# Kernel tuning notes

Measured on AMD Instinct MI355X. Metric: run time of the kernel, lower is better.

The kernel has to match this reference:

```python
import jax, jax.numpy as jnp
import numpy as np

N_NODES = 10000
N_EDGES = 80000
IN_DIM = 768
HID = 256
HEADS = 8
NEG_SLOPE = 0.2


def setup_inputs() -> dict:
    key = jax.random.key(0)
    ks = jax.random.split(key, 12)
    s = 0.02
    x = jax.random.normal(ks[0], (N_NODES, IN_DIM), dtype=jnp.float32)
    edge_index = jax.random.randint(ks[1], (2, N_EDGES), 0, N_NODES, dtype=jnp.int64)
    W1 = jax.random.normal(ks[2], (IN_DIM, HEADS * HID), dtype=jnp.float32) * s
    a_src1 = jax.random.normal(ks[3], (HEADS, HID), dtype=jnp.float32) * s
    a_dst1 = jax.random.normal(ks[4], (HEADS, HID), dtype=jnp.float32) * s
    b1 = jnp.zeros((HEADS * HID,), dtype=jnp.float32)
    W2 = jax.random.normal(ks[5], (HEADS * HID, HEADS * HID), dtype=jnp.float32) * s
    a_src2 = jax.random.normal(ks[6], (HEADS, HID), dtype=jnp.float32) * s
    a_dst2 = jax.random.normal(ks[7], (HEADS, HID), dtype=jnp.float32) * s
    b2 = jnp.zeros((HID,), dtype=jnp.float32)
    # graph_projection: 256 -> 256
    Wp = jax.random.normal(ks[8], (HID, HID), dtype=jnp.float32) * s
    bp = jnp.zeros((HID,), dtype=jnp.float32)
    return dict(x=x, edge_index=edge_index, W1=W1, a_src1=a_src1, a_dst1=a_dst1,
                b1=b1, W2=W2, a_src2=a_src2, a_dst2=a_dst2, b2=b2, Wp=Wp, bp=bp)


def _gat_conv(x, src, dst, W, a_src, a_dst, b, concat):
    """PyG GATConv (eval mode, self-loops already appended to src/dst)."""
    N = x.shape[0]
    H, C = a_src.shape
    h = (x @ W).reshape(N, H, C)                         # [N,H,C] per-head projection
    alpha_s = jnp.sum(h * a_src[None], axis=-1)           # [N,H]
    alpha_d = jnp.sum(h * a_dst[None], axis=-1)           # [N,H]
    e = jax.nn.leaky_relu(alpha_s[src] + alpha_d[dst], NEG_SLOPE)  # [E,H]
    # segment softmax over incoming edges of each dst node
    m = jax.ops.segment_max(e, dst, num_segments=N)       # [N,H]
    m = jnp.where(jnp.isfinite(m), m, 0.0)
    p = jnp.exp(e - m[dst])
    denom = jax.ops.segment_sum(p, dst, num_segments=N)   # [N,H]
    alpha = p / (denom[dst] + 1e-16)                      # [E,H]
    out = jax.ops.segment_sum(alpha[:, :, None] * h[src], dst, num_segments=N)  # [N,H,C]
    if concat:
        return out.reshape(N, H * C) + b
    return out.mean(axis=1) + b


def reference(x, edge_index, W1, a_src1, a_dst1, b1, W2, a_src2, a_dst2, b2, Wp, bp):
    N = x.shape[0]
    loops = jnp.arange(N, dtype=edge_index.dtype)
    src = jnp.concatenate([edge_index[0], loops])
    dst = jnp.concatenate([edge_index[1], loops])
    h = _gat_conv(x, src, dst, W1, a_src1, a_dst1, b1, concat=True)   # [N, 2048]
    h = jax.nn.elu(h)                                                 # dropout: eval/no-op
    h = _gat_conv(h, src, dst, W2, a_src2, a_dst2, b2, concat=False)  # [N, 256]
    h = h @ Wp + bp
    return jax.nn.relu(h)                                             # dropout: eval/no-op
```

## Files before the change

kernel.cpp:

```cpp
#include <hip/hip_runtime.h>
#include <cstdint>
#include <cstddef>

#define IN_DIM  768
#define NNODES  10000
#define MPAD    10112
#define NEDGES  80000
#define E_TOT   90000
#define HEADS   8
#define HID     256
#define HC      2048
#define NEG_SLOPE 0.2f

#define CVT_BLK  ((MPAD * IN_DIM / 4) / 256)
#define CNT_BLK  ((E_TOT + 255) / 256)
#define T1_BLK   ((HC / 32) * (IN_DIM / 32))
#define T2_BLK   ((HC / 32) * (HC / 32))
#define TP_BLK   ((HID / 32) * (HID / 32))
#define PREP_BLK (CVT_BLK + CNT_BLK + T1_BLK + T2_BLK + TP_BLK)

typedef _Float16 __attribute__((ext_vector_type(8))) f16x8;
typedef float    __attribute__((ext_vector_type(4))) f32x4;

__device__ __forceinline__ int edge_src(const int* __restrict__ ei, int e) {
    return (e < NEDGES) ? ei[e] : (e - NEDGES);
}
__device__ __forceinline__ int edge_dst(const int* __restrict__ ei, int e) {
    return (e < NEDGES) ? ei[NEDGES + e] : (e - NEDGES);
}

__device__ __forceinline__ void tcvt_body(
    const float* __restrict__ W, _Float16* __restrict__ T,
    int K, int N, int bx, int by, int t)
{
    __shared__ float tile[32][33];
    int tx = t & 31, ty = t >> 5;
#pragma unroll
    for (int q = 0; q < 4; q++)
        tile[ty + q * 8][tx] = W[(size_t)(by * 32 + ty + q * 8) * N + bx * 32 + tx];
    __syncthreads();
#pragma unroll
    for (int q = 0; q < 4; q++) {
        float v = tile[tx][ty + q * 8];
        T[(size_t)(bx * 32 + ty + q * 8) * K + by * 32 + tx] = (_Float16)v;
    }
}

__global__ __launch_bounds__(256) void prep_kernel(
    const float* __restrict__ x, _Float16* __restrict__ xh,
    const int* __restrict__ ei, int* __restrict__ cnt,
    const float* __restrict__ W1, _Float16* __restrict__ W1t,
    const float* __restrict__ W2, _Float16* __restrict__ W2t,
    const float* __restrict__ Wp, _Float16* __restrict__ Wpt)
{
    int b = blockIdx.x;
    int t = threadIdx.x;
    if (b < CVT_BLK) {
        int i = b * 256 + t;
        size_t e = (size_t)i * 4;
        int r = (int)(e / IN_DIM);
        float4 v = (r < NNODES) ? *(const float4*)(x + e)
                                : make_float4(0.f, 0.f, 0.f, 0.f);
        _Float16 h4[4] = {(_Float16)v.x, (_Float16)v.y, (_Float16)v.z, (_Float16)v.w};
        *(ushort4*)(xh + e) = *(ushort4*)h4;
    } else if (b < CVT_BLK + CNT_BLK) {
        int e = (b - CVT_BLK) * 256 + t;
        if (e < E_TOT) atomicAdd(&cnt[edge_dst(ei, e)], 1);
    } else if (b < CVT_BLK + CNT_BLK + T1_BLK) {
        int idx = b - (CVT_BLK + CNT_BLK);
        tcvt_body(W1, W1t, IN_DIM, HC, idx % (HC / 32), idx / (HC / 32), t);
    } else if (b < CVT_BLK + CNT_BLK + T1_BLK + T2_BLK) {
        int idx = b - (CVT_BLK + CNT_BLK + T1_BLK);
        tcvt_body(W2, W2t, HC, HC, idx % (HC / 32), idx / (HC / 32), t);
    } else {
        int idx = b - (CVT_BLK + CNT_BLK + T1_BLK + T2_BLK);
        tcvt_body(Wp, Wpt, HID, HID, idx % (HID / 32), idx / (HID / 32), t);
    }
}

__global__ void scan_kernel(const int* __restrict__ cnt, int* __restrict__ indptr) {
    __shared__ int sums[1024];
    const int CH = 10;
    int t = threadIdx.x;
    int base = t * CH;
    int s = 0;
#pragma unroll
    for (int i = 0; i < CH; i++) { int idx = base + i; if (idx < NNODES) s += cnt[idx]; }
    sums[t] = s;
    __syncthreads();
    for (int off = 1; off < 1024; off <<= 1) {
        int v = (t >= off) ? sums[t - off] : 0;
        __syncthreads();
        sums[t] += v;
        __syncthreads();
    }
    int run = (t == 0) ? 0 : sums[t - 1];
#pragma unroll
    for (int i = 0; i < CH; i++) {
        int idx = base + i;
        if (idx < NNODES) { indptr[idx] = run; run += cnt[idx]; }
    }
    if (t == 0) indptr[NNODES] = E_TOT;
}

__global__ void scatter_kernel(const int* __restrict__ ei, const int* __restrict__ indptr,
                               int* __restrict__ cur, int* __restrict__ sorted) {
    int e = blockIdx.x * 256 + threadIdx.x;
    if (e < E_TOT) {
        int d = edge_dst(ei, e);
        int pos = atomicAdd(&cur[d], 1);
        sorted[indptr[d] + pos] = e;
    }
}

template <int EPI>
__global__ __launch_bounds__(256) void mfma_gemm_kernel(
    const _Float16* __restrict__ A, const _Float16* __restrict__ B,
    void* __restrict__ Cout, const float* __restrict__ bias,
    int M, int K, int Nn, int swz)
{
    __shared__ __align__(16) _Float16 sA[2][128 * 32];
    __shared__ __align__(16) _Float16 sB[2][128 * 32];

    int t = threadIdx.x;
    int bx = blockIdx.x, by = blockIdx.y;
    if (swz) {
        int id = by * 16 + bx;
        int xcd = id & 7, slot = id >> 3;
        bx = 2 * xcd + (slot & 1);
        by = slot >> 1;
    }
    int row0 = by * 128;
    int col0 = bx * 128;

    int s0 = t, s1 = t + 256;
    int m0 = s0 >> 2, k0 = (s0 & 3) * 8;
    int m1 = s1 >> 2, k1 = (s1 & 3) * 8;
    const _Float16* a0 = A + (size_t)(row0 + m0) * K + k0;
    const _Float16* a1 = A + (size_t)(row0 + m1) * K + k1;
    const _Float16* b0 = B + (size_t)(col0 + m0) * K + k0;
    const _Float16* b1 = B + (size_t)(col0 + m1) * K + k1;

    int w = t >> 6, lane = t & 63;
    int wm = (w & 1) * 64, wn = (w >> 1) * 64;
    int fr = lane & 15, quad = lane >> 4;

    auto stage = [&](int kt, int bsel) {
        _Float16* dA0 = &sA[bsel][(w * 64) * 8];
        _Float16* dA1 = &sA[bsel][(w * 64 + 256) * 8];
        _Float16* dB0 = &sB[bsel][(w * 64) * 8];
        _Float16* dB1 = &sB[bsel][(w * 64 + 256) * 8];
        __builtin_amdgcn_global_load_lds(
            (const __attribute__((address_space(1))) void*)(a0 + kt),
            (__attribute__((address_space(3))) void*)dA0, 16, 0, 0);
        __builtin_amdgcn_global_load_lds(
            (const __attribute__((address_space(1))) void*)(a1 + kt),
            (__attribute__((address_space(3))) void*)dA1, 16, 0, 0);
        __builtin_amdgcn_global_load_lds(
            (const __attribute__((address_space(1))) void*)(b0 + kt),
            (__attribute__((address_space(3))) void*)dB0, 16, 0, 0);
        __builtin_amdgcn_global_load_lds(
            (const __attribute__((address_space(1))) void*)(b1 + kt),
            (__attribute__((address_space(3))) void*)dB1, 16, 0, 0);
    };

    f32x4 acc[4][4];
#pragma unroll
    for (int i = 0; i < 4; i++)
#pragma unroll
        for (int j = 0; j < 4; j++) acc[i][j] = {0.f, 0.f, 0.f, 0.f};

    const int nIt = K / 32;
    stage(0, 0);
    __syncthreads();

    for (int it = 0; it < nIt; ++it) {
        int cb = it & 1;
        if (it + 1 < nIt) stage((it + 1) * 32, cb ^ 1);

        f16x8 fa[4], fb[4];
#pragma unroll
        for (int i = 0; i < 4; i++) {
            fa[i] = *(const f16x8*)&sA[cb][(wm + i * 16 + fr) * 32 + quad * 8];
            fb[i] = *(const f16x8*)&sB[cb][(wn + i * 16 + fr) * 32 + quad * 8];
        }
#pragma unroll
        for (int i = 0; i < 4; i++)
#pragma unroll
            for (int j = 0; j < 4; j++)
                acc[i][j] = __builtin_amdgcn_mfma_f32_16x16x32_f16(fa[i], fb[j], acc[i][j], 0, 0, 0);

        if (it + 1 < nIt) __syncthreads();
    }

    if (EPI == 0) {
        _Float16* C = (_Float16*)Cout;
#pragma unroll
        for (int i = 0; i < 4; i++) {
            int mbase = row0 + wm + i * 16 + quad * 4;
#pragma unroll
            for (int j = 0; j < 4; j++) {
                int n = col0 + wn + j * 16 + fr;
#pragma unroll
                for (int r = 0; r < 4; r++) {
                    int m = mbase + r;
                    if (m < M) C[(size_t)m * Nn + n] = (_Float16)acc[i][j][r];
                }
            }
        }
    } else {
        float* C = (float*)Cout;
        float bv[4];
#pragma unroll
        for (int j = 0; j < 4; j++) bv[j] = bias[col0 + wn + j * 16 + fr];
#pragma unroll
        for (int i = 0; i < 4; i++) {
            int mbase = row0 + wm + i * 16 + quad * 4;
#pragma unroll
            for (int j = 0; j < 4; j++) {
                int n = col0 + wn + j * 16 + fr;
#pragma unroll
                for (int r = 0; r < 4; r++) {
                    int m = mbase + r;
                    if (m < M) C[(size_t)m * Nn + n] = fmaxf(acc[i][j][r] + bv[j], 0.f);
                }
            }
        }
    }
}

__global__ __launch_bounds__(256) void attn_kernel(
    const _Float16* __restrict__ H, const float* __restrict__ a_src,
    const float* __restrict__ a_dst, float* __restrict__ as_out,
    float* __restrict__ ad_out)
{
    int n = blockIdx.x;
    int t = threadIdx.x;
    int h = t >> 5, l = t & 31;
    f16x8 hv = *(const f16x8*)&H[(size_t)n * HC + h * HID + l * 8];
    const float* asp = a_src + h * HID + l * 8;
    const float* adp = a_dst + h * HID + l * 8;
    float sa = 0.f, sd = 0.f;
#pragma unroll
    for (int q = 0; q < 8; q++) {
        float v = (float)hv[q];
        sa = fmaf(v, asp[q], sa);
        sd = fmaf(v, adp[q], sd);
    }
#pragma unroll
    for (int o = 16; o > 0; o >>= 1) {
        sa += __shfl_xor(sa, o, 32);
        sd += __shfl_xor(sd, o, 32);
    }
    if (l == 0) { as_out[n * HEADS + h] = sa; ad_out[n * HEADS + h] = sd; }
}

template <int MODE>
__global__ __launch_bounds__(256) void agg_kernel(
    const _Float16* __restrict__ H, const float* __restrict__ as_,
    const float* __restrict__ ad_, const float* __restrict__ bias,
    const int* __restrict__ indptr, const int* __restrict__ sorted,
    const int* __restrict__ ei, _Float16* __restrict__ outh)
{
    __shared__ float m8[HEADS], d8[HEADS], adl[HEADS];
    __shared__ int   srcl[64];
    __shared__ float al[64][HEADS];
    __shared__ float red[HC];

    int n = blockIdx.x;
    int t = threadIdx.x;

    if (n >= NNODES) {
        if (MODE == 0) {
            _Float16 z8[8] = {};
            *(f16x8*)&outh[(size_t)n * HC + t * 8] = *(f16x8*)z8;
        } else {
            outh[(size_t)n * HID + t] = (_Float16)0.f;
        }
        return;
    }

    int start = indptr[n];
    int deg = indptr[n + 1] - start;

    if (t < HEADS) adl[t] = ad_[n * HEADS + t];
    __syncthreads();

    int h = t >> 5, l = t & 31;
    float adh = adl[h];

    float mx = -1e30f;
    for (int j = l; j < deg; j += 32) {
        int e = sorted[start + j];
        int s = edge_src(ei, e);
        float v = as_[s * HEADS + h] + adh;
        v = (v >= 0.f) ? v : NEG_SLOPE * v;
        mx = fmaxf(mx, v);
    }
#pragma unroll
    for (int o = 16; o > 0; o >>= 1) mx = fmaxf(mx, __shfl_xor(mx, o, 32));

    float sm = 0.f;
    for (int j = l; j < deg; j += 32) {
        int e = sorted[start + j];
        int s = edge_src(ei, e);
        float v = as_[s * HEADS + h] + adh;
        v = (v >= 0.f) ? v : NEG_SLOPE * v;
        sm += expf(v - mx);
    }
#pragma unroll
    for (int o = 16; o > 0; o >>= 1) sm += __shfl_xor(sm, o, 32);
    if (l == 0) { m8[h] = mx; d8[h] = sm; }

    int hh = t >> 5, c8 = (t & 31) * 8;
    const size_t hoff = (size_t)hh * HID + c8;
    float acc[8] = {};
    for (int base = 0; base < deg; base += 64) {
        int cntc = min(64, deg - base);
        __syncthreads();
        if (t < cntc) srcl[t] = edge_src(ei, sorted[start + base + t]);
        __syncthreads();
        {
            int j = t & 63, h0 = t >> 6;
            if (j < cntc) {
#pragma unroll
                for (int q = 0; q < 2; q++) {
                    int hx = h0 + q * 4;
                    float v = as_[srcl[j] * HEADS + hx] + adl[hx];
                    v = (v >= 0.f) ? v : NEG_SLOPE * v;
                    al[j][hx] = expf(v - m8[hx]) / (d8[hx] + 1e-16f);
                }
            }
        }
        __syncthreads();
        for (int jj = 0; jj < cntc; jj++) {
            int s = srcl[jj];
            f16x8 hv = *(const f16x8*)&H[(size_t)s * HC + hoff];
            float a = al[jj][hh];
#pragma unroll
            for (int q = 0; q < 8; q++)
                acc[q] = fmaf(a, (float)hv[q], acc[q]);
        }
    }

    if (MODE == 0) {
        _Float16 o8[8];
#pragma unroll
        for (int q = 0; q < 8; q++) {
            float v = acc[q] + bias[hoff + q];
            v = (v > 0.f) ? v : expm1f(v);
            o8[q] = (_Float16)v;
        }
        *(f16x8*)&outh[(size_t)n * HC + hoff] = *(f16x8*)o8;
    } else {
#pragma unroll
        for (int q = 0; q < 8; q++) red[hoff + q] = acc[q];
        __syncthreads();
        float s = 0.f;
#pragma unroll
        for (int h2 = 0; h2 < HEADS; h2++) s += red[h2 * HID + t];
        outh[(size_t)n * HID + t] = (_Float16)(s * 0.125f + bias[t]);
    }
}

extern "C" void kernel_launch(void* const* d_in, const int* in_sizes, int n_in,
                              void* d_out, int out_size, void* d_ws, size_t ws_size,
                              hipStream_t stream)
{
    const float* x      = (const float*)d_in[0];
    const int*   ei     = (const int*)  d_in[1];
    const float* W1     = (const float*)d_in[2];
    const float* a_src1 = (const float*)d_in[3];
    const float* a_dst1 = (const float*)d_in[4];
    const float* b1     = (const float*)d_in[5];
    const float* W2     = (const float*)d_in[6];
    const float* a_src2 = (const float*)d_in[7];
    const float* a_dst2 = (const float*)d_in[8];
    const float* b2     = (const float*)d_in[9];
    const float* Wp     = (const float*)d_in[10];
    const float* bp     = (const float*)d_in[11];
    float* out = (float*)d_out;

    char* ws = (char*)d_ws;
    size_t off = 0;
    auto alloc = [&](size_t bytes) -> char* {
        char* p = ws + off;
        off += (bytes + 255) & ~(size_t)255;
        return p;
    };
    _Float16* Hbuf = (_Float16*)alloc((size_t)NNODES * HC * 2);
    _Float16* A2   = (_Float16*)alloc((size_t)MPAD * HC * 2);
    _Float16* W1t  = (_Float16*)alloc((size_t)HC * IN_DIM * 2);
    _Float16* W2t  = (_Float16*)alloc((size_t)HC * HC * 2);
    _Float16* Wpt  = (_Float16*)alloc((size_t)HID * HID * 2);
    _Float16* xh   = (_Float16*)alloc((size_t)MPAD * IN_DIM * 2);
    _Float16* out2h = (_Float16*)alloc((size_t)MPAD * HID * 2);
    float* asad   = (float*)alloc((size_t)4 * NNODES * HEADS * sizeof(float));
    float* as1 = asad;
    float* ad1 = asad + (size_t)NNODES * HEADS;
    float* as2 = asad + (size_t)2 * NNODES * HEADS;
    float* ad2 = asad + (size_t)3 * NNODES * HEADS;
    int*   cntcur = (int*)alloc((size_t)2 * NNODES * sizeof(int));
    int*   cnt = cntcur;
    int*   cur = cntcur + NNODES;
    int*   indptr = (int*)  alloc((size_t)(NNODES + 1) * sizeof(int));
    int*   sorted = (int*)  alloc((size_t)E_TOT * sizeof(int));

    hipMemsetAsync(cntcur, 0, (size_t)2 * NNODES * sizeof(int), stream);
    prep_kernel<<<PREP_BLK, 256, 0, stream>>>(x, xh, ei, cnt,
                                              W1, W1t, W2, W2t, Wp, Wpt);
    scan_kernel<<<1, 1024, 0, stream>>>(cnt, indptr);
    scatter_kernel<<<(E_TOT + 255) / 256, 256, 0, stream>>>(ei, indptr, cur, sorted);

    dim3 gMf(HC / 128, MPAD / 128);

    mfma_gemm_kernel<0><<<gMf, 256, 0, stream>>>(xh, W1t, Hbuf, nullptr,
                                                 NNODES, IN_DIM, HC, 1);
    attn_kernel<<<NNODES, 256, 0, stream>>>(Hbuf, a_src1, a_dst1, as1, ad1);
    agg_kernel<0><<<MPAD, 256, 0, stream>>>(Hbuf, as1, ad1, b1, indptr, sorted, ei, A2);

    mfma_gemm_kernel<0><<<gMf, 256, 0, stream>>>(A2, W2t, Hbuf, nullptr,
                                                 NNODES, HC, HC, 1);
    attn_kernel<<<NNODES, 256, 0, stream>>>(Hbuf, a_src2, a_dst2, as2, ad2);
    agg_kernel<1><<<MPAD, 256, 0, stream>>>(Hbuf, as2, ad2, b2, indptr, sorted, ei, out2h);

    dim3 gProj(HID / 128, MPAD / 128);
    mfma_gemm_kernel<1><<<gProj, 256, 0, stream>>>(out2h, Wpt, out, bp,
                                                   NNODES, HID, HID, 0);
}
```

Measured before the change: 455.8 us.

## Fold attention-coefficient dot products into GEMM via precombined weight columns

Precomputes W·a_src and W·a_dst per head as 16 extra B-matrix rows (padded to a 128-column tile), so each GAT GEMM emits alpha_s/alpha_d in an extra column block and the separate attn_kernel passes over H are removed. The attention logits now come from fp16-rounded combined weights instead of dot products over the fp16 H, which shifts numerics slightly. It also drops the XCD block swizzle in the GEMM, and the extra column tile adds roughly 1/16 more GEMM blocks, mostly wasted MFMA work.

```diff
diff --git a/kernel.cpp b/kernel.cpp
--- a/kernel.cpp
+++ b/kernel.cpp
@@ -11,13 +11,19 @@
 #define HID     256
 #define HC      2048
 #define NEG_SLOPE 0.2f
+#define BROWS   (HC + 128)
 
 #define CVT_BLK  ((MPAD * IN_DIM / 4) / 256)
 #define CNT_BLK  ((E_TOT + 255) / 256)
 #define T1_BLK   ((HC / 32) * (IN_DIM / 32))
 #define T2_BLK   ((HC / 32) * (HC / 32))
 #define TP_BLK   ((HID / 32) * (HID / 32))
-#define PREP_BLK (CVT_BLK + CNT_BLK + T1_BLK + T2_BLK + TP_BLK)
+#define WC1_BLK  (16 * (IN_DIM / 128))
+#define WC2_BLK  (16 * (HC / 128))
+#define Z1_BLK   (112 * IN_DIM / 2048)
+#define Z2_BLK   (112 * HC / 2048)
+#define PREP_BLK (CVT_BLK + CNT_BLK + T1_BLK + T2_BLK + TP_BLK + \
+                  WC1_BLK + WC2_BLK + Z1_BLK + Z2_BLK)
 
 typedef _Float16 __attribute__((ext_vector_type(8))) f16x8;
 typedef float    __attribute__((ext_vector_type(4))) f32x4;
@@ -43,6 +49,28 @@
     for (int q = 0; q < 4; q++) {
         float v = tile[tx][ty + q * 8];
         T[(size_t)(bx * 32 + ty + q * 8) * K + by * 32 + tx] = (_Float16)v;
+    }
+}
+
+__device__ __forceinline__ void wcomb_body(
+    const float* __restrict__ W, const float* __restrict__ a,
+    _Float16* __restrict__ T, int K, int h16, int ktile, int t)
+{
+    int h = h16 & 7;
+    const float* av = a + h * HID;
+    int w = t >> 6, lane = t & 63;
+    float ar[4];
+#pragma unroll
+    for (int q = 0; q < 4; q++) ar[q] = av[lane + 64 * q];
+    for (int kk = w; kk < 128; kk += 4) {
+        int k = ktile * 128 + kk;
+        const float* wp = W + (size_t)k * HC + h * HID;
+        float s = 0.f;
+#pragma unroll
+        for (int q = 0; q < 4; q++) s = fmaf(wp[lane + 64 * q], ar[q], s);
+#pragma unroll
+        for (int o = 32; o > 0; o >>= 1) s += __shfl_xor(s, o, 64);
+        if (lane == 0) T[(size_t)(HC + h16) * K + k] = (_Float16)s;
     }
 }
 
@@ -51,11 +79,14 @@
     const int* __restrict__ ei, int* __restrict__ cnt,
     const float* __restrict__ W1, _Float16* __restrict__ W1t,
     const float* __restrict__ W2, _Float16* __restrict__ W2t,
-    const float* __restrict__ Wp, _Float16* __restrict__ Wpt)
+    const float* __restrict__ Wp, _Float16* __restrict__ Wpt,
+    const float* __restrict__ as1, const float* __restrict__ ad1,
+    const float* __restrict__ as2, const float* __restrict__ ad2)
 {
     int b = blockIdx.x;
     int t = threadIdx.x;
-    if (b < CVT_BLK) {
+    int base = 0;
+    if (b < (base += CVT_BLK)) {
         int i = b * 256 + t;
         size_t e = (size_t)i * 4;
         int r = (int)(e / IN_DIM);
@@ -63,18 +94,52 @@
                                 : make_float4(0.f, 0.f, 0.f, 0.f);
         _Float16 h4[4] = {(_Float16)v.x, (_Float16)v.y, (_Float16)v.z, (_Float16)v.w};
         *(ushort4*)(xh + e) = *(ushort4*)h4;
-    } else if (b < CVT_BLK + CNT_BLK) {
-        int e = (b - CVT_BLK) * 256 + t;
+        return;
+    }
+    if (b < (base += CNT_BLK)) {
+        int e = (b - (base - CNT_BLK)) * 256 + t;
         if (e < E_TOT) atomicAdd(&cnt[edge_dst(ei, e)], 1);
-    } else if (b < CVT_BLK + CNT_BLK + T1_BLK) {
-        int idx = b - (CVT_BLK + CNT_BLK);
+        return;
+    }
+    if (b < (base += T1_BLK)) {
+        int idx = b - (base - T1_BLK);
         tcvt_body(W1, W1t, IN_DIM, HC, idx % (HC / 32), idx / (HC / 32), t);
-    } else if (b < CVT_BLK + CNT_BLK + T1_BLK + T2_BLK) {
-        int idx = b - (CVT_BLK + CNT_BLK + T1_BLK);
+        return;
+    }
+    if (b < (base += T2_BLK)) {
+        int idx = b - (base - T2_BLK);
         tcvt_body(W2, W2t, HC, HC, idx % (HC / 32), idx / (HC / 32), t);
-    } else {
-        int idx = b - (CVT_BLK + CNT_BLK + T1_BLK + T2_BLK);
+        return;
+    }
+    if (b < (base += TP_BLK)) {
+        int idx = b - (base - TP_BLK);
         tcvt_body(Wp, Wpt, HID, HID, idx % (HID / 32), idx / (HID / 32), t);
+        return;
+    }
+    if (b < (base += WC1_BLK)) {
+        int idx = b - (base - WC1_BLK);
+        int h16 = idx / (IN_DIM / 128), ktile = idx % (IN_DIM / 128);
+        wcomb_body(W1, (h16 < 8) ? as1 : ad1, W1t, IN_DIM, h16, ktile, t);
+        return;
+    }
+    if (b < (base += WC2_BLK)) {
+        int idx = b - (base - WC2_BLK);
+        int h16 = idx / (HC / 128), ktile = idx % (HC / 128);
+        wcomb_body(W2, (h16 < 8) ? as2 : ad2, W2t, HC, h16, ktile, t);
+        return;
+    }
+    if (b < (base += Z1_BLK)) {
+        int idx = b - (base - Z1_BLK);
+        _Float16 z8[8] = {};
+        size_t e = (size_t)(HC + 16) * IN_DIM + (size_t)idx * 2048 + t * 8;
+        *(f16x8*)&W1t[e] = *(f16x8*)z8;
+        return;
+    }
+    {
+        int idx = b - base;
+        _Float16 z8[8] = {};
+        size_t e = (size_t)(HC + 16) * HC + (size_t)idx * 2048 + t * 8;
+        *(f16x8*)&W2t[e] = *(f16x8*)z8;
     }
 }
 
@@ -117,21 +182,14 @@
 __global__ __launch_bounds__(256) void mfma_gemm_kernel(
     const _Float16* __restrict__ A, const _Float16* __restrict__ B,
     void* __restrict__ Cout, const float* __restrict__ bias,
-    int M, int K, int Nn, int swz)
+    float* __restrict__ asad, int M, int K, int Nn)
 {
     __shared__ __align__(16) _Float16 sA[2][128 * 32];
     __shared__ __align__(16) _Float16 sB[2][128 * 32];
 
     int t = threadIdx.x;
-    int bx = blockIdx.x, by = blockIdx.y;
-    if (swz) {
-        int id = by * 16 + bx;
-        int xcd = id & 7, slot = id >> 3;
-        bx = 2 * xcd + (slot & 1);
-        by = slot >> 1;
-    }
-    int row0 = by * 128;
-    int col0 = bx * 128;
+    int row0 = blockIdx.y * 128;
+    int col0 = blockIdx.x * 128;
 
     int s0 = t, s1 = t + 256;
     int m0 = s0 >> 2, k0 = (s0 & 3) * 8;
@@ -193,6 +251,20 @@
         if (it + 1 < nIt) __syncthreads();
     }
 
+    if (EPI == 0 && col0 >= Nn) {
+        if (wn == 0) {
+#pragma unroll
+            for (int i = 0; i < 4; i++) {
+                int mbase = row0 + wm + i * 16 + quad * 4;
+#pragma unroll
+                for (int r = 0; r < 4; r++) {
+                    int m = mbase + r;
+                    if (m < M) asad[(size_t)m * 16 + fr] = acc[i][0][r];
+                }
+            }
+        }
+        return;
+    }
     if (EPI == 0) {
         _Float16* C = (_Float16*)Cout;
 #pragma unroll
@@ -229,36 +301,10 @@
     }
 }
 
-__global__ __launch_bounds__(256) void attn_kernel(
-    const _Float16* __restrict__ H, const float* __restrict__ a_src,
-    const float* __restrict__ a_dst, float* __restrict__ as_out,
-    float* __restrict__ ad_out)
-{
-    int n = blockIdx.x;
-    int t = threadIdx.x;
-    int h = t >> 5, l = t & 31;
-    f16x8 hv = *(const f16x8*)&H[(size_t)n * HC + h * HID + l * 8];
-    const float* asp = a_src + h * HID + l * 8;
-    const float* adp = a_dst + h * HID + l * 8;
-    float sa = 0.f, sd = 0.f;
-#pragma unroll
-    for (int q = 0; q < 8; q++) {
-        float v = (float)hv[q];
-        sa = fmaf(v, asp[q], sa);
-        sd = fmaf(v, adp[q], sd);
-    }
-#pragma unroll
-    for (int o = 16; o > 0; o >>= 1) {
-        sa += __shfl_xor(sa, o, 32);
-        sd += __shfl_xor(sd, o, 32);
-    }
-    if (l == 0) { as_out[n * HEADS + h] = sa; ad_out[n * HEADS + h] = sd; }
-}
-
 template <int MODE>
 __global__ __launch_bounds__(256) void agg_kernel(
-    const _Float16* __restrict__ H, const float* __restrict__ as_,
-    const float* __restrict__ ad_, const float* __restrict__ bias,
+    const _Float16* __restrict__ H, const float* __restrict__ asad,
+    const float* __restrict__ bias,
     const int* __restrict__ indptr, const int* __restrict__ sorted,
     const int* __restrict__ ei, _Float16* __restrict__ outh)
 {
@@ -283,7 +329,7 @@
     int start = indptr[n];
     int deg = indptr[n + 1] - start;
 
-    if (t < HEADS) adl[t] = ad_[n * HEADS + t];
+    if (t < HEADS) adl[t] = asad[(size_t)n * 16 + 8 + t];
     __syncthreads();
 
     int h = t >> 5, l = t & 31;
@@ -293,7 +339,7 @@
     for (int j = l; j < deg; j += 32) {
         int e = sorted[start + j];
         int s = edge_src(ei, e);
-        float v = as_[s * HEADS + h] + adh;
+        float v = asad[(size_t)s * 16 + h] + adh;
         v = (v >= 0.f) ? v : NEG_SLOPE * v;
         mx = fmaxf(mx, v);
     }
@@ -304,7 +350,7 @@
     for (int j = l; j < deg; j += 32) {
         int e = sorted[start + j];
         int s = edge_src(ei, e);
-        float v = as_[s * HEADS + h] + adh;
+        float v = asad[(size_t)s * 16 + h] + adh;
         v = (v >= 0.f) ? v : NEG_SLOPE * v;
         sm += expf(v - mx);
     }
@@ -326,7 +372,7 @@
 #pragma unroll
                 for (int q = 0; q < 2; q++) {
                     int hx = h0 + q * 4;
-                    float v = as_[srcl[j] * HEADS + hx] + adl[hx];
+                    float v = asad[(size_t)srcl[j] * 16 + hx] + adl[hx];
                     v = (v >= 0.f) ? v : NEG_SLOPE * v;
                     al[j][hx] = expf(v - m8[hx]) / (d8[hx] + 1e-16f);
                 }
@@ -390,16 +436,13 @@
     };
     _Float16* Hbuf = (_Float16*)alloc((size_t)NNODES * HC * 2);
     _Float16* A2   = (_Float16*)alloc((size_t)MPAD * HC * 2);
-    _Float16* W1t  = (_Float16*)alloc((size_t)HC * IN_DIM * 2);
-    _Float16* W2t  = (_Float16*)alloc((size_t)HC * HC * 2);
+    _Float16* W1t  = (_Float16*)alloc((size_t)BROWS * IN_DIM * 2);
+    _Float16* W2t  = (_Float16*)alloc((size_t)BROWS * HC * 2);
     _Float16* Wpt  = (_Float16*)alloc((size_t)HID * HID * 2);
     _Float16* xh   = (_Float16*)alloc((size_t)MPAD * IN_DIM * 2);
     _Float16* out2h = (_Float16*)alloc((size_t)MPAD * HID * 2);
-    float* asad   = (float*)alloc((size_t)4 * NNODES * HEADS * sizeof(float));
-    float* as1 = asad;
-    float* ad1 = asad + (size_t)NNODES * HEADS;
-    float* as2 = asad + (size_t)2 * NNODES * HEADS;
-    float* ad2 = asad + (size_t)3 * NNODES * HEADS;
+    float* asad1 = (float*)alloc((size_t)MPAD * 16 * sizeof(float));
+    float* asad2 = (float*)alloc((size_t)MPAD * 16 * sizeof(float));
     int*   cntcur = (int*)alloc((size_t)2 * NNODES * sizeof(int));
     int*   cnt = cntcur;
     int*   cur = cntcur + NNODES;
@@ -408,23 +451,22 @@
 
     hipMemsetAsync(cntcur, 0, (size_t)2 * NNODES * sizeof(int), stream);
     prep_kernel<<<PREP_BLK, 256, 0, stream>>>(x, xh, ei, cnt,
-                                              W1, W1t, W2, W2t, Wp, Wpt);
+                                              W1, W1t, W2, W2t, Wp, Wpt,
+                                              a_src1, a_dst1, a_src2, a_dst2);
     scan_kernel<<<1, 1024, 0, stream>>>(cnt, indptr);
     scatter_kernel<<<(E_TOT + 255) / 256, 256, 0, stream>>>(ei, indptr, cur, sorted);
 
-    dim3 gMf(HC / 128, MPAD / 128);
+    dim3 gMf(HC / 128 + 1, MPAD / 128);
 
     mfma_gemm_kernel<0><<<gMf, 256, 0, stream>>>(xh, W1t, Hbuf, nullptr,
-                                                 NNODES, IN_DIM, HC, 1);
-    attn_kernel<<<NNODES, 256, 0, stream>>>(Hbuf, a_src1, a_dst1, as1, ad1);
-    agg_kernel<0><<<MPAD, 256, 0, stream>>>(Hbuf, as1, ad1, b1, indptr, sorted, ei, A2);
+                                                 asad1, NNODES, IN_DIM, HC);
+    agg_kernel<0><<<MPAD, 256, 0, stream>>>(Hbuf, asad1, b1, indptr, sorted, ei, A2);
 
     mfma_gemm_kernel<0><<<gMf, 256, 0, stream>>>(A2, W2t, Hbuf, nullptr,
-                                                 NNODES, HC, HC, 1);
-    attn_kernel<<<NNODES, 256, 0, stream>>>(Hbuf, a_src2, a_dst2, as2, ad2);
-    agg_kernel<1><<<MPAD, 256, 0, stream>>>(Hbuf, as2, ad2, b2, indptr, sorted, ei, out2h);
+                                                 asad2, NNODES, HC, HC);
+    agg_kernel<1><<<MPAD, 256, 0, stream>>>(Hbuf, asad2, b2, indptr, sorted, ei, out2h);
 
     dim3 gProj(HID / 128, MPAD / 128);
     mfma_gemm_kernel<1><<<gProj, 256, 0, stream>>>(out2h, Wpt, out, bp,
-                                                   NNODES, HID, HID, 0);
-}
+                                                   nullptr, NNODES, HID, HID);
+}
```

After: 473.5 us. +3.9%, slower.
